# Performance work log

Hardware: AMD Instinct MI355X
Metric: run time of the kernel (lower is better)

## Reference

```python
import jax, jax.numpy as jnp
import numpy as np

CODE_DIM = 256
CODEBOOK_SIZE = 8192
N = 32768
BETA = 0.25


def setup_inputs() -> dict:
    key = jax.random.key(0)
    k1, k2 = jax.random.split(key)
    z = jax.random.normal(k1, (N, CODE_DIM), dtype=jnp.float32)
    # nn.Embedding weight init: uniform(-1/code_dim, 1/code_dim)
    codebook = jax.random.uniform(
        k2, (CODEBOOK_SIZE, CODE_DIM), dtype=jnp.float32,
        minval=-1.0 / CODE_DIM, maxval=1.0 / CODE_DIM)
    return {"z": z, "codebook": codebook}


def reference(z, codebook):
    # z: (N, D) already flat (z.view(N, -1) in torch). codebook: (K, D)
    # squared euclidean distances via expansion: ||z||^2 - 2 z.E^T + ||E||^2
    z_sq = jnp.sum(z * z, axis=1, keepdims=True)            # (N, 1)
    e_sq = jnp.sum(codebook * codebook, axis=1)             # (K,)
    dist = z_sq - 2.0 * (z @ codebook.T) + e_sq[None, :]    # (N, K)
    indices = jnp.argmin(dist, axis=1)                      # (N,)
    z_q = codebook[indices]                                 # (N, D)

    commitment_loss = jnp.mean((jax.lax.stop_gradient(z_q) - z) ** 2)
    codebook_loss = jnp.mean((z_q - jax.lax.stop_gradient(z)) ** 2)
    loss = BETA * commitment_loss + codebook_loss

    # straight-through estimator
    z_q_ste = z + jax.lax.stop_gradient(z_q - z)
    return (z_q_ste, loss)
```

## Files before the change

### kernel.cpp

```cpp
#include <hip/hip_runtime.h>
#include <cfloat>

#define NROWS  32768
#define NCODES 8192
#define DDIM   256
#define KG     4
#define CPB    (NCODES / KG)
#define CT     64
#define TPB    (CPB / CT)
#define RPB    256

typedef __attribute__((ext_vector_type(8)))  __bf16 bf16x8;
typedef __attribute__((ext_vector_type(16))) float  f32x16;

__global__ __launch_bounds__(256)
void cvt_cb(const float* __restrict__ cb, __bf16* __restrict__ cbb,
            float* __restrict__ esq) {
    const size_t i = (size_t)(blockIdx.x * 256 + threadIdx.x) * 8;
    const float4 f0 = *(const float4*)(cb + i);
    const float4 f1 = *(const float4*)(cb + i + 4);
    bf16x8 v;
    v[0] = (__bf16)f0.x; v[1] = (__bf16)f0.y; v[2] = (__bf16)f0.z; v[3] = (__bf16)f0.w;
    v[4] = (__bf16)f1.x; v[5] = (__bf16)f1.y; v[6] = (__bf16)f1.z; v[7] = (__bf16)f1.w;
    *(bf16x8*)(cbb + i) = v;
    float s = f0.x * f0.x + f0.y * f0.y + f0.z * f0.z + f0.w * f0.w
            + f1.x * f1.x + f1.y * f1.y + f1.z * f1.z + f1.w * f1.w;
    for (int o = 16; o > 0; o >>= 1) s += __shfl_down(s, o, 32);
    if ((threadIdx.x & 31) == 0) esq[i >> 8] = s + 1.0f;
}

__global__ __launch_bounds__(256, 2)
void vq_mfma(const float* __restrict__ z, const __bf16* __restrict__ cbb,
             const float* __restrict__ esq, unsigned* __restrict__ pK) {
    __shared__ __align__(16) __bf16 Bb[2][CT * DDIM];

    const int rowbase  = (blockIdx.x >> 2) * RPB;
    const int kg       = blockIdx.x & 3;
    const int codebase = kg * CPB;

    const int tid = threadIdx.x;
    const int w = tid >> 6, l = tid & 63;
    const int la = l & 31, lh = l >> 5;
    const int loff = la * DDIM + lh * 8;

#pragma unroll
    for (int jj = 0; jj < 8; ++jj) {
        const int p = w * 8 + jj;
        const int fc = p >> 4, kc = p & 15;
        __builtin_amdgcn_global_load_lds(
            (const __attribute__((address_space(1))) void*)
                (cbb + (size_t)(codebase + fc * 32) * DDIM + kc * 16 + loff),
            (__attribute__((address_space(3))) void*)(&Bb[0][p * 512]),
            16, 0, 0);
    }

    bf16x8 Af[2][16];
    {
        const float* zp = z + (size_t)(rowbase + w * 64 + la) * DDIM + lh * 8;
#pragma unroll
        for (int s = 0; s < 2; ++s)
#pragma unroll
            for (int kc = 0; kc < 16; ++kc) {
                const float4 f0 = *(const float4*)(zp + s * 32 * DDIM + kc * 16);
                const float4 f1 = *(const float4*)(zp + s * 32 * DDIM + kc * 16 + 4);
                bf16x8 v;
                v[0] = (__bf16)(-2.f * f0.x); v[1] = (__bf16)(-2.f * f0.y);
                v[2] = (__bf16)(-2.f * f0.z); v[3] = (__bf16)(-2.f * f0.w);
                v[4] = (__bf16)(-2.f * f1.x); v[5] = (__bf16)(-2.f * f1.y);
                v[6] = (__bf16)(-2.f * f1.z); v[7] = (__bf16)(-2.f * f1.w);
                Af[s][kc] = v;
            }
    }

    float evc[2], evn[2];
    evc[0] = esq[codebase + la];
    evc[1] = esq[codebase + 32 + la];

    unsigned bestK[32];
#pragma unroll
    for (int s = 0; s < 32; ++s) bestK[s] = 0xFFFFFFFFu;

    __syncthreads();

    int buf = 0;
#pragma unroll 1
    for (int t = 0; t < TPB; ++t) {
        if (t + 1 < TPB) {
            const __bf16* base = cbb + (size_t)(codebase + (t + 1) * CT) * DDIM;
#pragma unroll
            for (int jj = 0; jj < 8; ++jj) {
                const int p = w * 8 + jj;
                const int fc = p >> 4, kc = p & 15;
                __builtin_amdgcn_global_load_lds(
                    (const __attribute__((address_space(1))) void*)
                        (base + (size_t)(fc * 32) * DDIM + kc * 16 + loff),
                    (__attribute__((address_space(3))) void*)(&Bb[buf ^ 1][p * 512]),
                    16, 0, 0);
            }
        }
        {
            const int tn = (t + 1) & (TPB - 1);
            evn[0] = esq[codebase + tn * CT + la];
            evn[1] = esq[codebase + tn * CT + 32 + la];
        }

        const __bf16* Bc = &Bb[buf][0];

        f32x16 acc0, acc1;
#pragma unroll
        for (int r = 0; r < 16; ++r) { acc0[r] = evc[0]; acc1[r] = evc[0]; }
        __builtin_amdgcn_s_setprio(1);
#pragma unroll
        for (int kc = 0; kc < 16; ++kc) {
            const bf16x8 b = *(const bf16x8*)(Bc + kc * 512 + l * 8);
            acc0 = __builtin_amdgcn_mfma_f32_32x32x16_bf16(Af[0][kc], b, acc0, 0, 0, 0);
            acc1 = __builtin_amdgcn_mfma_f32_32x32x16_bf16(Af[1][kc], b, acc1, 0, 0, 0);
        }
        __builtin_amdgcn_s_setprio(0);
        {
            const unsigned cA = (unsigned)(codebase + t * CT + la);
#pragma unroll
            for (int r = 0; r < 16; ++r) {
                const unsigned k0 = (__float_as_uint(acc0[r]) & 0xFFFFE000u) | cA;
                if (k0 < bestK[r])      bestK[r]      = k0;
                const unsigned k1 = (__float_as_uint(acc1[r]) & 0xFFFFE000u) | cA;
                if (k1 < bestK[16 + r]) bestK[16 + r] = k1;
            }
        }

#pragma unroll
        for (int r = 0; r < 16; ++r) { acc0[r] = evc[1]; acc1[r] = evc[1]; }
        __builtin_amdgcn_s_setprio(1);
#pragma unroll
        for (int kc = 0; kc < 16; ++kc) {
            const bf16x8 b = *(const bf16x8*)(Bc + (16 + kc) * 512 + l * 8);
            acc0 = __builtin_amdgcn_mfma_f32_32x32x16_bf16(Af[0][kc], b, acc0, 0, 0, 0);
            acc1 = __builtin_amdgcn_mfma_f32_32x32x16_bf16(Af[1][kc], b, acc1, 0, 0, 0);
        }
        __builtin_amdgcn_s_setprio(0);
        {
            const unsigned cB = (unsigned)(codebase + t * CT + 32 + la);
#pragma unroll
            for (int r = 0; r < 16; ++r) {
                const unsigned k0 = (__float_as_uint(acc0[r]) & 0xFFFFE000u) | cB;
                if (k0 < bestK[r])      bestK[r]      = k0;
                const unsigned k1 = (__float_as_uint(acc1[r]) & 0xFFFFE000u) | cB;
                if (k1 < bestK[16 + r]) bestK[16 + r] = k1;
            }
        }

        evc[0] = evn[0]; evc[1] = evn[1];

        __syncthreads();
        buf ^= 1;
    }

#pragma unroll
    for (int s = 0; s < 32; ++s) {
#pragma unroll
        for (int m = 1; m < 32; m <<= 1) {
            const unsigned k2 = (unsigned)__shfl_xor((int)bestK[s], m);
            if (k2 < bestK[s]) bestK[s] = k2;
        }
    }
    if (la == 0) {
#pragma unroll
        for (int s = 0; s < 2; ++s)
#pragma unroll
            for (int r = 0; r < 16; ++r) {
                const int rl = w * 64 + s * 32 + (r & 3) + 8 * (r >> 2) + 4 * lh;
                pK[(size_t)(rowbase + rl) * KG + kg] = bestK[s * 16 + r];
            }
    }
}

__global__ __launch_bounds__(256)
void vq_finalize(const float* __restrict__ z, const float* __restrict__ cb,
                 const unsigned* __restrict__ pK,
                 float* __restrict__ out, float* __restrict__ bsum) {
    __shared__ float sSum[4];
    __shared__ int   sIdx[4];
    const int tid = threadIdx.x;
    const int rw = tid >> 6, lane = tid & 63;
    const int row = blockIdx.x * 4 + rw;

    if (lane == 0) {
        unsigned k = pK[row * KG];
#pragma unroll
        for (int q = 1; q < KG; ++q) {
            const unsigned k2 = pK[row * KG + q];
            if (k2 < k) k = k2;
        }
        sIdx[rw] = (int)(k & 0x1FFFu);
    }
    __syncthreads();
    const int idx = sIdx[rw];

    const float4 zv = *(const float4*)(z  + (size_t)row * DDIM + lane * 4);
    const float4 ev = *(const float4*)(cb + (size_t)idx * DDIM + lane * 4);
    float4 d, o;
    d.x = ev.x - zv.x; d.y = ev.y - zv.y; d.z = ev.z - zv.z; d.w = ev.w - zv.w;
    o.x = zv.x + d.x;  o.y = zv.y + d.y;  o.z = zv.z + d.z;  o.w = zv.w + d.w;
    *(float4*)(out + (size_t)row * DDIM + lane * 4) = o;

    float s = d.x * d.x + d.y * d.y + d.z * d.z + d.w * d.w;
    for (int off = 32; off > 0; off >>= 1) s += __shfl_down(s, off);
    if (lane == 0) sSum[rw] = s;
    __syncthreads();
    if (tid == 0) bsum[blockIdx.x] = sSum[0] + sSum[1] + sSum[2] + sSum[3];
}

__global__ __launch_bounds__(256)
void loss_final(const float* __restrict__ bsum, float* __restrict__ out) {
    __shared__ float red[4];
    const int tid = threadIdx.x;
    float s = 0.f;
    for (int i = tid; i < NROWS / 4; i += 256) s += bsum[i];
    for (int off = 32; off > 0; off >>= 1) s += __shfl_down(s, off);
    const int wv = tid >> 6, lane = tid & 63;
    if (lane == 0) red[wv] = s;
    __syncthreads();
    if (tid == 0) {
        const float tot = red[0] + red[1] + red[2] + red[3];
        out[(size_t)NROWS * DDIM] = tot * (1.25f / (float)((size_t)NROWS * DDIM));
    }
}

extern "C" void kernel_launch(void* const* d_in, const int* in_sizes, int n_in,
                              void* d_out, int out_size, void* d_ws, size_t ws_size,
                              hipStream_t stream) {
    const float* z  = (const float*)d_in[0];
    const float* cb = (const float*)d_in[1];
    float* out = (float*)d_out;

    __bf16* cbf = (__bf16*)d_out;

    float*    esq  = (float*)d_ws;
    unsigned* pK   = (unsigned*)(esq + NCODES);
    float*    bsum = (float*)(pK + NROWS * KG);

    cvt_cb<<<NCODES * DDIM / 8 / 256, 256, 0, stream>>>(cb, cbf, esq);
    vq_mfma<<<(NROWS / RPB) * KG, 256, 0, stream>>>(z, cbf, esq, pK);
    vq_finalize<<<NROWS / 4, 256, 0, stream>>>(z, cb, pK, out, bsum);
    loss_final<<<1, 256, 0, stream>>>(bsum, out);
}
```

Measured before the change: 236.7 us.

## Software-pipeline argmin epilogue behind MFMA chains across tile halves

Splits each tile's two MFMA accumulator sets into P and Q, and defers the argmin scan of the second half (Q) to the next iteration so it sits after the next P MFMA chain. The goal is to hide the VALU compare/min work behind in-flight MFMA latency rather than serializing it after each chain. A dummy initial Q accumulator (value 2.0) is scanned harmlessly in the first iteration, and a tail scan after the loop handles the last Q. This costs 32 more live accumulator VGPRs, which risks spills or lower occupancy.

```diff
diff --git a/kernel.cpp b/kernel.cpp
--- a/kernel.cpp
+++ b/kernel.cpp
@@ -80,11 +80,47 @@
 #pragma unroll
     for (int s = 0; s < 32; ++s) bestK[s] = 0xFFFFFFFFu;
 
+    f32x16 accQ0, accQ1;
+#pragma unroll
+    for (int r = 0; r < 16; ++r) { accQ0[r] = 2.f; accQ1[r] = 2.f; }
+    unsigned pQcol = (unsigned)codebase;
+
     __syncthreads();
 
     int buf = 0;
 #pragma unroll 1
     for (int t = 0; t < TPB; ++t) {
+        const __bf16* Bc = &Bb[buf][0];
+
+        f32x16 einit;
+#pragma unroll
+        for (int r = 0; r < 16; ++r) einit[r] = evc[0];
+        f32x16 accP0, accP1;
+        __builtin_amdgcn_s_setprio(1);
+        {
+            const bf16x8 b = *(const bf16x8*)(Bc + l * 8);
+            accP0 = __builtin_amdgcn_mfma_f32_32x32x16_bf16(Af[0][0], b, einit, 0, 0, 0);
+            accP1 = __builtin_amdgcn_mfma_f32_32x32x16_bf16(Af[1][0], b, einit, 0, 0, 0);
+        }
+#pragma unroll
+        for (int kc = 1; kc < 16; ++kc) {
+            const bf16x8 b = *(const bf16x8*)(Bc + kc * 512 + l * 8);
+            accP0 = __builtin_amdgcn_mfma_f32_32x32x16_bf16(Af[0][kc], b, accP0, 0, 0, 0);
+            accP1 = __builtin_amdgcn_mfma_f32_32x32x16_bf16(Af[1][kc], b, accP1, 0, 0, 0);
+        }
+        __builtin_amdgcn_s_setprio(0);
+
+        {
+            const unsigned cQ = pQcol + (unsigned)la;
+#pragma unroll
+            for (int r = 0; r < 16; ++r) {
+                const unsigned k0 = (__float_as_uint(accQ0[r]) & 0xFFFFE000u) | cQ;
+                if (k0 < bestK[r])      bestK[r]      = k0;
+                const unsigned k1 = (__float_as_uint(accQ1[r]) & 0xFFFFE000u) | cQ;
+                if (k1 < bestK[16 + r]) bestK[16 + r] = k1;
+            }
+        }
+
         if (t + 1 < TPB) {
             const __bf16* base = cbb + (size_t)(codebase + (t + 1) * CT) * DDIM;
 #pragma unroll
@@ -104,47 +140,30 @@
             evn[1] = esq[codebase + tn * CT + 32 + la];
         }
 
-        const __bf16* Bc = &Bb[buf][0];
-
-        f32x16 acc0, acc1;
-#pragma unroll
-        for (int r = 0; r < 16; ++r) { acc0[r] = evc[0]; acc1[r] = evc[0]; }
+#pragma unroll
+        for (int r = 0; r < 16; ++r) einit[r] = evc[1];
         __builtin_amdgcn_s_setprio(1);
-#pragma unroll
-        for (int kc = 0; kc < 16; ++kc) {
-            const bf16x8 b = *(const bf16x8*)(Bc + kc * 512 + l * 8);
-            acc0 = __builtin_amdgcn_mfma_f32_32x32x16_bf16(Af[0][kc], b, acc0, 0, 0, 0);
-            acc1 = __builtin_amdgcn_mfma_f32_32x32x16_bf16(Af[1][kc], b, acc1, 0, 0, 0);
+        {
+            const bf16x8 b = *(const bf16x8*)(Bc + 16 * 512 + l * 8);
+            accQ0 = __builtin_amdgcn_mfma_f32_32x32x16_bf16(Af[0][0], b, einit, 0, 0, 0);
+            accQ1 = __builtin_amdgcn_mfma_f32_32x32x16_bf16(Af[1][0], b, einit, 0, 0, 0);
+        }
+#pragma unroll
+        for (int kc = 1; kc < 16; ++kc) {
+            const bf16x8 b = *(const bf16x8*)(Bc + (16 + kc) * 512 + l * 8);
+            accQ0 = __builtin_amdgcn_mfma_f32_32x32x16_bf16(Af[0][kc], b, accQ0, 0, 0, 0);
+            accQ1 = __builtin_amdgcn_mfma_f32_32x32x16_bf16(Af[1][kc], b, accQ1, 0, 0, 0);
         }
         __builtin_amdgcn_s_setprio(0);
-        {
-            const unsigned cA = (unsigned)(codebase + t * CT + la);
+        pQcol = (unsigned)(codebase + t * CT + 32);
+
+        {
+            const unsigned cP = (unsigned)(codebase + t * CT + la);
 #pragma unroll
             for (int r = 0; r < 16; ++r) {
-                const unsigned k0 = (__float_as_uint(acc0[r]) & 0xFFFFE000u) | cA;
+                const unsigned k0 = (__float_as_uint(accP0[r]) & 0xFFFFE000u) | cP;
                 if (k0 < bestK[r])      bestK[r]      = k0;
-                const unsigned k1 = (__float_as_uint(acc1[r]) & 0xFFFFE000u) | cA;
-                if (k1 < bestK[16 + r]) bestK[16 + r] = k1;
-            }
-        }
-
-#pragma unroll
-        for (int r = 0; r < 16; ++r) { acc0[r] = evc[1]; acc1[r] = evc[1]; }
-        __builtin_amdgcn_s_setprio(1);
-#pragma unroll
-        for (int kc = 0; kc < 16; ++kc) {
-            const bf16x8 b = *(const bf16x8*)(Bc + (16 + kc) * 512 + l * 8);
-            acc0 = __builtin_amdgcn_mfma_f32_32x32x16_bf16(Af[0][kc], b, acc0, 0, 0, 0);
-            acc1 = __builtin_amdgcn_mfma_f32_32x32x16_bf16(Af[1][kc], b, acc1, 0, 0, 0);
-        }
-        __builtin_amdgcn_s_setprio(0);
-        {
-            const unsigned cB = (unsigned)(codebase + t * CT + 32 + la);
-#pragma unroll
-            for (int r = 0; r < 16; ++r) {
-                const unsigned k0 = (__float_as_uint(acc0[r]) & 0xFFFFE000u) | cB;
-                if (k0 < bestK[r])      bestK[r]      = k0;
-                const unsigned k1 = (__float_as_uint(acc1[r]) & 0xFFFFE000u) | cB;
+                const unsigned k1 = (__float_as_uint(accP1[r]) & 0xFFFFE000u) | cP;
                 if (k1 < bestK[16 + r]) bestK[16 + r] = k1;
             }
         }
@@ -153,6 +172,17 @@
 
         __syncthreads();
         buf ^= 1;
+    }
+
+    {
+        const unsigned cQ = pQcol + (unsigned)la;
+#pragma unroll
+        for (int r = 0; r < 16; ++r) {
+            const unsigned k0 = (__float_as_uint(accQ0[r]) & 0xFFFFE000u) | cQ;
+            if (k0 < bestK[r])      bestK[r]      = k0;
+            const unsigned k1 = (__float_as_uint(accQ1[r]) & 0xFFFFE000u) | cQ;
+            if (k1 < bestK[16 + r]) bestK[16 + r] = k1;
+        }
     }
 
 #pragma unroll
```

After: 603.1 us. +154.8%, slower.
